# Kernel tuning notes

Measured on AMD Instinct MI355X. Metric: run time of the kernel, lower is better.

Reference implementation:

```python
import jax, jax.numpy as jnp
import numpy as np

IGNORE_INDEX = -100


def setup_inputs() -> dict:
    key = jax.random.key(0)
    k1, k2, k3 = jax.random.split(key, 3)
    B, S, D, V = 2, 4096, 2048, 32000
    outputs = jax.random.normal(k1, (B, S, D), dtype=jnp.float32)
    # LM-head weight, nn.Linear convention: [vocab, embed_dim], scaled like typical init
    weight = jax.random.normal(k2, (V, D), dtype=jnp.float32) * (D ** -0.5)
    targets = jax.random.randint(k3, (B, S), 0, V, dtype=jnp.int64)
    return {"outputs": outputs, "weight": weight, "targets": targets}


def reference(outputs, weight, targets):
    # Flatten tokens: [B, S, D] -> [N, D], [B, S] -> [N]
    D = outputs.shape[-1]
    x = outputs.reshape(-1, D)            # [N, D]
    t = targets.reshape(-1)               # [N]
    # Fused linear projection: logits [N, V]
    logits = jnp.einsum("nd,vd->nv", x, weight)
    logp = jax.nn.log_softmax(logits, axis=-1)
    valid = t != IGNORE_INDEX
    safe_t = jnp.where(valid, t, 0)
    # Gather target log-prob per token
    nll = -jnp.take_along_axis(logp, safe_t[:, None], axis=1)[:, 0]  # [N]
    n_valid = jnp.maximum(jnp.sum(valid.astype(nll.dtype)), 1.0)
    loss = jnp.sum(jnp.where(valid, nll, 0.0)) / n_valid
    return loss
```

## Files before the change

kernel.cpp:

```cpp
#include <hip/hip_runtime.h>
#include <hip/hip_bf16.h>
#include <math.h>

#define IGNORE_INDEX (-100)

typedef __attribute__((ext_vector_type(4))) float f32x4;

static const int NTOK = 2 * 4096;
static const int DIM  = 2048;
static const int VOC  = 32000;
static const int BM = 256, BN = 256;
static const int KS = 64;
static const int NPH = DIM / KS;
static const int NVT = VOC / BN;
static const int MT  = NTOK / BM;
static const float WSCALE = 16.0f;


__device__ inline void gload_lds16(const void* g, void* l) {
  __builtin_amdgcn_global_load_lds(
      (const __attribute__((address_space(1))) void*)g,
      (__attribute__((address_space(3))) void*)l,
      16, 0, 0);
}


__global__ void cast_f32_fp8(const float* __restrict__ in,
                             unsigned char* __restrict__ out, long n8, float scale) {
  long i0 = (long)blockIdx.x * blockDim.x + threadIdx.x;
  long stride = (long)gridDim.x * blockDim.x;
  for (long i = i0; i < n8; i += stride) {
    const float4* p = (const float4*)(in + i * 8);
    float4 a = p[0], b = p[1];
    int lo = __builtin_amdgcn_cvt_pk_fp8_f32(a.x * scale, a.y * scale, 0, false);
    lo = __builtin_amdgcn_cvt_pk_fp8_f32(a.z * scale, a.w * scale, lo, true);
    int hi = __builtin_amdgcn_cvt_pk_fp8_f32(b.x * scale, b.y * scale, 0, false);
    hi = __builtin_amdgcn_cvt_pk_fp8_f32(b.z * scale, b.w * scale, hi, true);
    int2 o; o.x = lo; o.y = hi;
    *(int2*)(out + i * 8) = o;
  }
}


#define VM8  asm volatile("s_waitcnt vmcnt(8)" ::: "memory")
#define VM4  asm volatile("s_waitcnt vmcnt(4)" ::: "memory")
#define VM0  asm volatile("s_waitcnt vmcnt(0)" ::: "memory")
#define BARRIER asm volatile("s_barrier" ::: "memory")

#define STAGE(SLOT) do { \
  char* _dA = stA + (SLOT) * 16384; \
  char* _dB = stB + (SLOT) * 16384; \
  gload_lds16(aCur, _dA); \
  gload_lds16(aCur + 32, _dA + 8192); \
  gload_lds16(bCur, _dB); \
  gload_lds16(bCur + 32, _dB + 8192); \
  aCur += KS; bCur += KS; \
} while (0)

__launch_bounds__(512, 2)
__global__ void lce_gemm(const unsigned char* __restrict__ xq,
                         const unsigned char* __restrict__ wq,
                         float* __restrict__ pmax, float* __restrict__ psum) {
  extern __shared__ char smem[];
  char* smA = smem;
  char* smB = smem + 65536;

  const int nwg = NVT * MT;
  const int cpx = nwg >> 3;
  const int bid = blockIdx.x;
  const int swz = (bid & 7) * cpx + (bid >> 3);
  const int vt = swz / MT;
  const int mt = swz % MT;
  const int m0 = mt * BM;
  const int v0 = vt * BN;

  const int tid = threadIdx.x;
  const int lane = tid & 63;
  const int w = tid >> 6;
  const int wr = w >> 2, wc = w & 3;
  const int li = lane & 15, lg = lane >> 4;

  f32x4 acc[8][4];
  const f32x4 z = {0.f, 0.f, 0.f, 0.f};
#pragma unroll
  for (int i = 0; i < 8; ++i)
#pragma unroll
    for (int j = 0; j < 4; ++j) acc[i][j] = z;

  const int floc = lane >> 5;
  const int li_s = (lane >> 1) & 15;
  const int u_s = lane & 1;
  const int kb = ((u_s ^ (li_s >> 3)) << 4);
  const int rowoff = 32 * w + 16 * floc + li_s;
  const unsigned char* aCur = xq + (long)(m0 + rowoff) * DIM + kb;
  const unsigned char* bCur = wq + (long)(v0 + rowoff) * DIM + kb;
  char* stA = smA + w * 1024;
  char* stB = smB + w * 1024;

  const int lgs = (lg ^ ((li >> 3) << 1));
  const int aLane = li * 32 + lgs * 8;
  const char* aRd = smA + wr * 4096 + aLane;
  const char* bRd = smB + wc * 2048 + aLane;

  STAGE(0);
  STAGE(1);
  STAGE(2);
  VM8;
  BARRIER;

#pragma unroll 1
  for (int n = 0; n < NPH; ++n) {
    const int slot = n & 3;
    const char* Ab = aRd + slot * 16384;
    const char* Bb = bRd + slot * 16384;

    long a0[8], a1[8], b0[4], b1[4];
#pragma unroll
    for (int i = 0; i < 8; ++i) a0[i] = *(const long*)(Ab + i * 512);
#pragma unroll
    for (int j = 0; j < 4; ++j) b0[j] = *(const long*)(Bb + j * 512);
#pragma unroll
    for (int i = 0; i < 8; ++i) a1[i] = *(const long*)(Ab + 8192 + i * 512);
#pragma unroll
    for (int j = 0; j < 4; ++j) b1[j] = *(const long*)(Bb + 8192 + j * 512);

    if (n < NPH - 3) STAGE(((n + 3) & 3));
    BARRIER;
    __builtin_amdgcn_s_setprio(1);
#pragma unroll
    for (int i = 0; i < 8; ++i)
#pragma unroll
      for (int j = 0; j < 4; ++j)
        acc[i][j] = __builtin_amdgcn_mfma_f32_16x16x32_fp8_fp8(a0[i], b0[j], acc[i][j], 0, 0, 0);
#pragma unroll
    for (int i = 0; i < 8; ++i)
#pragma unroll
      for (int j = 0; j < 4; ++j)
        acc[i][j] = __builtin_amdgcn_mfma_f32_16x16x32_fp8_fp8(a1[i], b1[j], acc[i][j], 0, 0, 0);
    __builtin_amdgcn_s_setprio(0);
    if (n < NPH - 3) { VM8; }
    else if (n == NPH - 3) { VM4; }
    else if (n == NPH - 2) { VM0; }
    BARRIER;
  }

  const float sc = 1.0f / WSCALE;
  float* sm_m = (float*)smem;
  float* sm_s = (float*)(smem + 4096);
  __syncthreads();
#pragma unroll
  for (int i = 0; i < 8; ++i) {
#pragma unroll
    for (int r = 0; r < 4; ++r) {
      float l0 = acc[i][0][r] * sc, l1 = acc[i][1][r] * sc;
      float l2 = acc[i][2][r] * sc, l3 = acc[i][3][r] * sc;
      float m = fmaxf(fmaxf(l0, l1), fmaxf(l2, l3));
#pragma unroll
      for (int mk = 1; mk < 16; mk <<= 1) m = fmaxf(m, __shfl_xor(m, mk));
      float s = __expf(l0 - m) + __expf(l1 - m) + __expf(l2 - m) + __expf(l3 - m);
#pragma unroll
      for (int mk = 1; mk < 16; mk <<= 1) s += __shfl_xor(s, mk);
      if (li == 0) {
        int R = wr * 128 + i * 16 + lg * 4 + r;
        sm_m[wc * 256 + R] = m;
        sm_s[wc * 256 + R] = s;
      }
    }
  }
  __syncthreads();
  if (tid < BM) {
    float ma = sm_m[tid], mb = sm_m[256 + tid], mc = sm_m[512 + tid], md = sm_m[768 + tid];
    float gm = fmaxf(fmaxf(ma, mb), fmaxf(mc, md));
    float gs = sm_s[tid] * __expf(ma - gm) + sm_s[256 + tid] * __expf(mb - gm) +
               sm_s[512 + tid] * __expf(mc - gm) + sm_s[768 + tid] * __expf(md - gm);
    long row = (long)(m0 + tid);
    pmax[row * NVT + vt] = gm;
    psum[row * NVT + vt] = gs;
  }
}


__global__ void token_reduce(const float* __restrict__ x, const float* __restrict__ wgt,
                             const int* __restrict__ tgt,
                             const float* __restrict__ pmax, const float* __restrict__ psum,
                             float* __restrict__ nll, float* __restrict__ validf) {
  const int n = blockIdx.x;
  const int tid = threadIdx.x;
  const int lane = tid & 63;
  const int w = tid >> 6;
  __shared__ float smr[4];

  const int t = tgt[n];
  const bool valid = (t != IGNORE_INDEX);
  const int ts = valid ? t : 0;

  const float4* xr = (const float4*)(x + (long)n * DIM);
  const float4* wr = (const float4*)(wgt + (long)ts * DIM);
  float d = 0.f;
  for (int i = tid; i < DIM / 4; i += blockDim.x) {
    float4 a = xr[i], b = wr[i];
    d += a.x * b.x + a.y * b.y + a.z * b.z + a.w * b.w;
  }

  float m = (tid < NVT) ? pmax[(long)n * NVT + tid] : -INFINITY;
  float t1 = m;
#pragma unroll
  for (int mk = 1; mk < 64; mk <<= 1) t1 = fmaxf(t1, __shfl_xor(t1, mk));
  if (lane == 0) smr[w] = t1;
  __syncthreads();
  const float gm = fmaxf(fmaxf(smr[0], smr[1]), fmaxf(smr[2], smr[3]));
  __syncthreads();

  float se = (tid < NVT) ? psum[(long)n * NVT + tid] * __expf(m - gm) : 0.f;
#pragma unroll
  for (int mk = 1; mk < 64; mk <<= 1) se += __shfl_xor(se, mk);
  if (lane == 0) smr[w] = se;
  __syncthreads();
  const float gs = smr[0] + smr[1] + smr[2] + smr[3];
  __syncthreads();

#pragma unroll
  for (int mk = 1; mk < 64; mk <<= 1) d += __shfl_xor(d, mk);
  if (lane == 0) smr[w] = d;
  __syncthreads();
  const float gd = smr[0] + smr[1] + smr[2] + smr[3];

  if (tid == 0) {
    nll[n] = valid ? (gm + logf(gs) - gd) : 0.f;
    validf[n] = valid ? 1.f : 0.f;
  }
}


__global__ void final_reduce(const float* __restrict__ nll, const float* __restrict__ validf,
                             float* __restrict__ out, int n) {
  const int tid = threadIdx.x;
  const int lane = tid & 63;
  const int w = tid >> 6;
  __shared__ float sm1[4], sm2[4];
  float s = 0.f, c = 0.f;
  for (int i = tid; i < n; i += blockDim.x) { s += nll[i]; c += validf[i]; }
#pragma unroll
  for (int mk = 1; mk < 64; mk <<= 1) { s += __shfl_xor(s, mk); c += __shfl_xor(c, mk); }
  if (lane == 0) { sm1[w] = s; sm2[w] = c; }
  __syncthreads();
  if (tid == 0) {
    float ts = sm1[0] + sm1[1] + sm1[2] + sm1[3];
    float tc = sm2[0] + sm2[1] + sm2[2] + sm2[3];
    out[0] = ts / fmaxf(tc, 1.0f);
  }
}


extern "C" void kernel_launch(void* const* d_in, const int* in_sizes, int n_in,
                              void* d_out, int out_size, void* d_ws, size_t ws_size,
                              hipStream_t stream) {
  const float* x = (const float*)d_in[0];
  const float* wgt = (const float*)d_in[1];
  const int* tgt = (const int*)d_in[2];
  float* out = (float*)d_out;

  char* ws = (char*)d_ws;
  const size_t xq_off = 0;
  const size_t wq_off = (size_t)NTOK * DIM;
  const size_t pm_off = wq_off + (size_t)VOC * DIM;
  const size_t ps_off = pm_off + (size_t)NTOK * NVT * 4;
  const size_t nl_off = ps_off + (size_t)NTOK * NVT * 4;
  const size_t vf_off = nl_off + (size_t)NTOK * 4;
  const size_t needed = vf_off + (size_t)NTOK * 4;
  if (ws_size < needed) return;

  unsigned char* xq = (unsigned char*)(ws + xq_off);
  unsigned char* wq = (unsigned char*)(ws + wq_off);
  float* pmax = (float*)(ws + pm_off);
  float* psum = (float*)(ws + ps_off);
  float* nllv = (float*)(ws + nl_off);
  float* vldf = (float*)(ws + vf_off);

  cast_f32_fp8<<<2048, 256, 0, stream>>>(x, xq, (long)NTOK * DIM / 8, 1.0f);
  cast_f32_fp8<<<4096, 256, 0, stream>>>(wgt, wq, (long)VOC * DIM / 8, WSCALE);

  (void)hipFuncSetAttribute((const void*)lce_gemm,
                            hipFuncAttributeMaxDynamicSharedMemorySize, 131072);
  lce_gemm<<<NVT * MT, 512, 131072, stream>>>(xq, wq, pmax, psum);

  token_reduce<<<NTOK, 256, 0, stream>>>(x, wgt, tgt, pmax, psum, nllv, vldf);
  final_reduce<<<1, 256, 0, stream>>>(nllv, vldf, out, NTOK);
}
```

Baseline: 1.138 ms.

## Interleave LDS reads, global-to-LDS staging and MFMA in four sub-phases

Changes the shared-memory layout so each lane reads 16-byte vectors holding both K halves contiguously, replacing the XOR-swizzled 8-byte reads. The main loop is split into four sub-phases. Each sub-phase loads a pair of A fragments, issues one global-to-LDS stage load and then runs 16 MFMAs, so LDS reads, staging and compute interleave at finer grain and register pressure drops. In exchange it adds many more barriers per iteration. Dropping the swizzle may bring back LDS bank conflicts.

```diff
diff --git a/kernel.cpp b/kernel.cpp
--- a/kernel.cpp
+++ b/kernel.cpp
@@ -5,6 +5,7 @@
 #define IGNORE_INDEX (-100)
 
 typedef __attribute__((ext_vector_type(4))) float f32x4;
+typedef __attribute__((ext_vector_type(2))) long lx2;
 
 static const int NTOK = 2 * 4096;
 static const int DIM  = 2048;
@@ -46,15 +47,11 @@
 #define VM4  asm volatile("s_waitcnt vmcnt(4)" ::: "memory")
 #define VM0  asm volatile("s_waitcnt vmcnt(0)" ::: "memory")
 #define BARRIER asm volatile("s_barrier" ::: "memory")
-
-#define STAGE(SLOT) do { \
-  char* _dA = stA + (SLOT) * 16384; \
-  char* _dB = stB + (SLOT) * 16384; \
-  gload_lds16(aCur, _dA); \
-  gload_lds16(aCur + 32, _dA + 8192); \
-  gload_lds16(bCur, _dB); \
-  gload_lds16(bCur + 32, _dB + 8192); \
-  aCur += KS; bCur += KS; \
+#define LGKM0 asm volatile("s_waitcnt lgkmcnt(0)" ::: "memory")
+
+#define MM2(ii, jj, AR, BR) do { \
+  acc[ii][jj] = __builtin_amdgcn_mfma_f32_16x16x32_fp8_fp8(AR[0], BR[0], acc[ii][jj], 0, 0, 0); \
+  acc[ii][jj] = __builtin_amdgcn_mfma_f32_16x16x32_fp8_fp8(AR[1], BR[1], acc[ii][jj], 0, 0, 0); \
 } while (0)
 
 __launch_bounds__(512, 2)
@@ -87,56 +84,75 @@
 #pragma unroll
     for (int j = 0; j < 4; ++j) acc[i][j] = z;
 
-  const int floc = lane >> 5;
-  const int li_s = (lane >> 1) & 15;
-  const int u_s = lane & 1;
-  const int kb = ((u_s ^ (li_s >> 3)) << 4);
-  const int rowoff = 32 * w + 16 * floc + li_s;
-  const unsigned char* aCur = xq + (long)(m0 + rowoff) * DIM + kb;
-  const unsigned char* bCur = wq + (long)(v0 + rowoff) * DIM + kb;
-  char* stA = smA + w * 1024;
-  char* stB = smB + w * 1024;
-
-  const int lgs = (lg ^ ((li >> 3) << 1));
-  const int aLane = li * 32 + lgs * 8;
-  const char* aRd = smA + wr * 4096 + aLane;
-  const char* bRd = smB + wc * 2048 + aLane;
-
-  STAGE(0);
-  STAGE(1);
-  STAGE(2);
+  const unsigned char* aS0 = xq + (long)(m0 + 2 * w * 16 + li) * DIM + lg * 16;
+  const unsigned char* aS1 = xq + (long)(m0 + (2 * w + 1) * 16 + li) * DIM + lg * 16;
+  const unsigned char* bS0 = wq + (long)(v0 + 2 * w * 16 + li) * DIM + lg * 16;
+  const unsigned char* bS1 = wq + (long)(v0 + (2 * w + 1) * 16 + li) * DIM + lg * 16;
+  char* stA = smA + 2 * w * 1024;
+  char* stB = smB + 2 * w * 1024;
+
+  const char* aRd = smA + wr * 8192 + lane * 16;
+  const char* bRd = smB + wc * 4096 + lane * 16;
+
+#pragma unroll
+  for (int s = 0; s < 3; ++s) {
+    gload_lds16(aS0, stA + s * 16384);        aS0 += KS;
+    gload_lds16(aS1, stA + s * 16384 + 1024); aS1 += KS;
+    gload_lds16(bS0, stB + s * 16384);        bS0 += KS;
+    gload_lds16(bS1, stB + s * 16384 + 1024); bS1 += KS;
+  }
   VM8;
   BARRIER;
 
 #pragma unroll 1
   for (int n = 0; n < NPH; ++n) {
     const int slot = n & 3;
+    const int dst = (n + 3) & 3;
     const char* Ab = aRd + slot * 16384;
     const char* Bb = bRd + slot * 16384;
-
-    long a0[8], a1[8], b0[4], b1[4];
-#pragma unroll
-    for (int i = 0; i < 8; ++i) a0[i] = *(const long*)(Ab + i * 512);
-#pragma unroll
-    for (int j = 0; j < 4; ++j) b0[j] = *(const long*)(Bb + j * 512);
-#pragma unroll
-    for (int i = 0; i < 8; ++i) a1[i] = *(const long*)(Ab + 8192 + i * 512);
-#pragma unroll
-    for (int j = 0; j < 4; ++j) b1[j] = *(const long*)(Bb + 8192 + j * 512);
-
-    if (n < NPH - 3) STAGE(((n + 3) & 3));
+    const bool stg = (n < NPH - 3);
+
+    lx2 B0 = *(const lx2*)(Bb);
+    lx2 B1 = *(const lx2*)(Bb + 1024);
+    lx2 B2 = *(const lx2*)(Bb + 2048);
+    lx2 B3 = *(const lx2*)(Bb + 3072);
+    lx2 A0 = *(const lx2*)(Ab);
+    lx2 A1 = *(const lx2*)(Ab + 1024);
+    if (stg) { gload_lds16(aS0, stA + dst * 16384); aS0 += KS; }
+    BARRIER; LGKM0;
+    __builtin_amdgcn_s_setprio(1);
+    MM2(0, 0, A0, B0); MM2(0, 1, A0, B1); MM2(0, 2, A0, B2); MM2(0, 3, A0, B3);
+    MM2(1, 0, A1, B0); MM2(1, 1, A1, B1); MM2(1, 2, A1, B2); MM2(1, 3, A1, B3);
+    __builtin_amdgcn_s_setprio(0);
     BARRIER;
+
+    A0 = *(const lx2*)(Ab + 2048);
+    A1 = *(const lx2*)(Ab + 3072);
+    if (stg) { gload_lds16(aS1, stA + dst * 16384 + 1024); aS1 += KS; }
+    BARRIER; LGKM0;
     __builtin_amdgcn_s_setprio(1);
-#pragma unroll
-    for (int i = 0; i < 8; ++i)
-#pragma unroll
-      for (int j = 0; j < 4; ++j)
-        acc[i][j] = __builtin_amdgcn_mfma_f32_16x16x32_fp8_fp8(a0[i], b0[j], acc[i][j], 0, 0, 0);
-#pragma unroll
-    for (int i = 0; i < 8; ++i)
-#pragma unroll
-      for (int j = 0; j < 4; ++j)
-        acc[i][j] = __builtin_amdgcn_mfma_f32_16x16x32_fp8_fp8(a1[i], b1[j], acc[i][j], 0, 0, 0);
+    MM2(2, 0, A0, B0); MM2(2, 1, A0, B1); MM2(2, 2, A0, B2); MM2(2, 3, A0, B3);
+    MM2(3, 0, A1, B0); MM2(3, 1, A1, B1); MM2(3, 2, A1, B2); MM2(3, 3, A1, B3);
+    __builtin_amdgcn_s_setprio(0);
+    BARRIER;
+
+    A0 = *(const lx2*)(Ab + 4096);
+    A1 = *(const lx2*)(Ab + 5120);
+    if (stg) { gload_lds16(bS0, stB + dst * 16384); bS0 += KS; }
+    BARRIER; LGKM0;
+    __builtin_amdgcn_s_setprio(1);
+    MM2(4, 0, A0, B0); MM2(4, 1, A0, B1); MM2(4, 2, A0, B2); MM2(4, 3, A0, B3);
+    MM2(5, 0, A1, B0); MM2(5, 1, A1, B1); MM2(5, 2, A1, B2); MM2(5, 3, A1, B3);
+    __builtin_amdgcn_s_setprio(0);
+    BARRIER;
+
+    A0 = *(const lx2*)(Ab + 6144);
+    A1 = *(const lx2*)(Ab + 7168);
+    if (stg) { gload_lds16(bS1, stB + dst * 16384 + 1024); bS1 += KS; }
+    BARRIER; LGKM0;
+    __builtin_amdgcn_s_setprio(1);
+    MM2(6, 0, A0, B0); MM2(6, 1, A0, B1); MM2(6, 2, A0, B2); MM2(6, 3, A0, B3);
+    MM2(7, 0, A1, B0); MM2(7, 1, A1, B1); MM2(7, 2, A1, B2); MM2(7, 3, A1, B3);
     __builtin_amdgcn_s_setprio(0);
     if (n < NPH - 3) { VM8; }
     else if (n == NPH - 3) { VM4; }
```

Result: faster. 959.9 us (-15.7%).
